# Performance work log

Measured on AMD Instinct MI355X. Metric: run time of the kernel, lower is better.

The kernel has to match this reference:

```python
import jax, jax.numpy as jnp
import numpy as np

N, E, G = 10000, 160000, 64     # nodes, edges, graphs in batch
T, F_IN, F_OUT, L = 5, 75, 15, 4  # towers, per-tower in (divide_input=False), per-tower out, conv layers
AVG_DEG_LOG = float(np.log(17.0))  # stand-in for PyG histogram stat (source deg=zeros -> NaN)
BN_EPS = 1e-5
STD_EPS = 1e-5


def _u(key, shape):
    fi, fo = shape[-2], shape[-1]
    lim = float(np.sqrt(6.0 / (fi + fo)))
    return jax.random.uniform(key, shape, jnp.float32, -lim, lim)


def setup_inputs():
    key = jax.random.key(0)
    k = iter(jax.random.split(key, 24))
    inp = {}
    inp["x"] = jax.random.randint(next(k), (N, 2), 0, 21)
    inp["edge_index"] = jax.random.randint(next(k), (2, E), 0, N)
    inp["edge_attr"] = jax.random.randint(next(k), (E, 2), 0, 4)
    inp["batch"] = jnp.sort(jax.random.randint(next(k), (N,), 0, G))
    inp["node_emb"] = jax.random.normal(next(k), (21, 75), jnp.float32)
    inp["edge_emb"] = jax.random.normal(next(k), (4, 25), jnp.float32)
    inp["pre_lin_W"] = _u(next(k), (150, 75)); inp["pre_lin_b"] = jnp.zeros((75,), jnp.float32)
    inp["edge_enc_W"] = _u(next(k), (L, 50, F_IN)); inp["edge_enc_b"] = jnp.zeros((L, F_IN), jnp.float32)
    inp["pre_W"] = _u(next(k), (L, T, 3 * F_IN, F_IN)); inp["pre_b"] = jnp.zeros((L, T, F_IN), jnp.float32)
    inp["post_W"] = _u(next(k), (L, T, 13 * F_IN, F_OUT)); inp["post_b"] = jnp.zeros((L, T, F_OUT), jnp.float32)
    inp["lin_W"] = _u(next(k), (L, T * F_OUT, 75)); inp["lin_b"] = jnp.zeros((L, 75), jnp.float32)
    inp["bn_g"] = jnp.ones((L, 75), jnp.float32); inp["bn_b"] = jnp.zeros((L, 75), jnp.float32)
    inp["mlp_W1"] = _u(next(k), (75, 50)); inp["mlp_b1"] = jnp.zeros((50,), jnp.float32)
    inp["mlp_W2"] = _u(next(k), (50, 25)); inp["mlp_b2"] = jnp.zeros((25,), jnp.float32)
    inp["mlp_W3"] = _u(next(k), (25, 1)); inp["mlp_b3"] = jnp.zeros((1,), jnp.float32)
    return inp


def _forward(x, edge_index, edge_attr, batch, node_emb, edge_emb, pre_lin_W, pre_lin_b,
             edge_enc_W, edge_enc_b, pre_W, pre_b, post_W, post_b, lin_W, lin_b,
             bn_g, bn_b, mlp_W1, mlp_b1, mlp_W2, mlp_b2, mlp_W3, mlp_b3):
    # node / edge embeddings -> features
    h = node_emb[x].reshape(N, 150) @ pre_lin_W + pre_lin_b          # [N,75]
    ea = edge_emb[edge_attr].reshape(E, 50)                           # [E,50]
    src, dst = edge_index[0], edge_index[1]  # messages flow src -> dst (x_j=src, x_i=dst)

    cnt = jax.ops.segment_sum(jnp.ones((E,), jnp.float32), dst, num_segments=N)  # in-degree [N]
    deg = jnp.maximum(cnt, 1.0)[:, None, None]
    log_deg = jnp.log(jnp.maximum(cnt, 1.0) + 1.0)[:, None, None]
    amp = log_deg / AVG_DEG_LOG
    att = AVG_DEG_LOG / log_deg
    has = (cnt > 0)[:, None, None]

    for l in range(L):
        e = ea @ edge_enc_W[l] + edge_enc_b[l]                        # [E,75]
        m_in = jnp.concatenate([h[dst], h[src], e], axis=-1)          # [E,225]
        msgs = jnp.einsum('ec,tcf->etf', m_in, pre_W[l]) + pre_b[l]   # [E,T,75]
        s = jax.ops.segment_sum(msgs, dst, num_segments=N)
        mean = s / deg
        mean_sq = jax.ops.segment_sum(msgs * msgs, dst, num_segments=N) / deg
        std = jnp.sqrt(jax.nn.relu(mean_sq - mean * mean) + STD_EPS)
        mn = jnp.where(has, jax.ops.segment_min(msgs, dst, num_segments=N), 0.0)
        mx = jnp.where(has, jax.ops.segment_max(msgs, dst, num_segments=N), 0.0)
        agg = jnp.concatenate([mean, mn, mx, std], axis=-1)           # [N,T,300]
        scaled = jnp.concatenate([agg, agg * amp, agg * att], axis=-1)  # [N,T,900]
        out = jnp.concatenate([jnp.broadcast_to(h[:, None, :], (N, T, F_IN)), scaled], axis=-1)  # [N,T,975]
        post = jnp.einsum('ntc,tcf->ntf', out, post_W[l]) + post_b[l]  # [N,T,15]
        hc = post.reshape(N, T * F_OUT) @ lin_W[l] + lin_b[l]          # [N,75]
        mu = hc.mean(axis=0)
        var = hc.var(axis=0)  # biased, matches BatchNorm1d training mode
        h = jax.nn.relu((hc - mu) / jnp.sqrt(var + BN_EPS) * bn_g[l] + bn_b[l])

    g = jax.ops.segment_sum(h, batch, num_segments=G)                 # global_add_pool [G,75]
    g = jax.nn.relu(g @ mlp_W1 + mlp_b1)
    g = jax.nn.relu(g @ mlp_W2 + mlp_b2)
    return g @ mlp_W3 + mlp_b3                                        # [G,1]


def reference(x, edge_index, edge_attr, batch, node_emb, edge_emb, pre_lin_W, pre_lin_b,
              edge_enc_W, edge_enc_b, pre_W, pre_b, post_W, post_b, lin_W, lin_b,
              bn_g, bn_b, mlp_W1, mlp_b1, mlp_W2, mlp_b2, mlp_W3, mlp_b3):
    return _forward(x, edge_index, edge_attr, batch, node_emb, edge_emb, pre_lin_W, pre_lin_b,
                    edge_enc_W, edge_enc_b, pre_W, pre_b, post_W, post_b, lin_W, lin_b,
                    bn_g, bn_b, mlp_W1, mlp_b1, mlp_W2, mlp_b2, mlp_W3, mlp_b3)
```

## Files before the change

### kernel.cpp

```cpp
#include <hip/hip_runtime.h>
#include <hip/hip_bf16.h>
#include <math.h>

#define NN 10000
#define NE 160000
#define NG 64
#define NT 5
#define NL 4
#define ADL 2.833213344056216f
#define AROW 1632

typedef __attribute__((ext_vector_type(8))) short bf16x8;
typedef __attribute__((ext_vector_type(4))) float f32x4;

#define OFF_H      0
#define OFF_HC     750000
#define OFF_P      1500000
#define OFF_Q      5250000
#define OFF_A      9000000
#define OFF_BT     17200000
#define OFF_BIASC  17400000
#define OFF_RLUT   24000000
#define OFF_INVDEG 24006000
#define OFF_AMP    24016000
#define OFF_ATT    24026000
#define OFF_STATS  24036000
#define OFF_GPOOL  24036160
#define OFF_INT    24118960

__device__ __forceinline__ float bf2f(__hip_bfloat16 v){ return __bfloat162float(v); }

__global__ void k_zero_cnt(int* cnt){
    int i = blockIdx.x*256 + threadIdx.x;
    if (i < NN) cnt[i] = 0;
}

__global__ void k_zpad(__hip_bfloat16* __restrict__ A){
    int idx = blockIdx.x*256 + threadIdx.x;
    if (idx >= NN*57) return;
    int n = idx/57, c = idx - n*57;
    int k = (c < 36) ? 1500 + c : 1611 + (c - 36);
    A[(size_t)n*AROW + k] = __float2bfloat16(0.f);
}

__global__ __launch_bounds__(256) void k_h0(const int* __restrict__ x,
        const float* __restrict__ node_emb, const float* __restrict__ plW,
        const float* __restrict__ plb, float* __restrict__ h,
        __hip_bfloat16* __restrict__ A){
    __shared__ float s_emb[21*75];
    __shared__ float s_W[150*75];
    __shared__ float s_b[75];
    int tid = threadIdx.x;
    for (int i = tid; i < 21*75; i += 256) s_emb[i] = node_emb[i];
    for (int i = tid; i < 150*75; i += 256) s_W[i] = plW[i];
    if (tid < 75) s_b[tid] = plb[tid];
    __syncthreads();
    for (int out = blockIdx.x*256 + tid; out < NN*75; out += gridDim.x*256){
        int n = out / 75, f = out - n*75;
        int x0 = x[2*n], x1 = x[2*n+1];
        float acc = s_b[f];
        const float* e0 = s_emb + x0*75;
        const float* e1 = s_emb + x1*75;
        #pragma unroll 5
        for (int k = 0; k < 75; k++)
            acc += e0[k]*s_W[k*75+f] + e1[k]*s_W[(75+k)*75+f];
        h[out] = acc;
        A[(size_t)n*AROW + 1536 + f] = __float2bfloat16(acc);
    }
}

__global__ void k_hist(const int* __restrict__ ei, int* __restrict__ cnt){
    int e = blockIdx.x*256 + threadIdx.x;
    if (e < NE) atomicAdd(&cnt[ei[NE + e]], 1);
}

__global__ void k_scan(const int* __restrict__ cnt, int* __restrict__ eoff){
    __shared__ int buf[256];
    __shared__ int carry;
    int tid = threadIdx.x;
    if (tid == 0){ carry = 0; eoff[0] = 0; }
    __syncthreads();
    for (int base = 0; base < NN; base += 256){
        int v = (base + tid < NN) ? cnt[base + tid] : 0;
        buf[tid] = v; __syncthreads();
        for (int off = 1; off < 256; off <<= 1){
            int t2 = (tid >= off) ? buf[tid - off] : 0;
            __syncthreads();
            buf[tid] += t2;
            __syncthreads();
        }
        int inc = buf[tid] + carry;
        if (base + tid < NN) eoff[base + tid + 1] = inc;
        __syncthreads();
        if (tid == 255) carry = inc;
        __syncthreads();
    }
}

__global__ void k_nodestats(const int* __restrict__ cnt, const int* __restrict__ eoff,
        float* __restrict__ invdeg, float* __restrict__ amp, float* __restrict__ att,
        int* __restrict__ cursor){
    int n = blockIdx.x*256 + threadIdx.x;
    if (n >= NN) return;
    int c = cnt[n];
    cursor[n] = eoff[n];
    float cf = (float)c;
    float dg = cf < 1.f ? 1.f : cf;
    invdeg[n] = 1.f / dg;
    float ld = logf(dg + 1.f);
    amp[n] = ld / ADL;
    att[n] = ADL / ld;
}

__global__ void k_scatter(const int* __restrict__ ei, const int* __restrict__ ea,
        int* __restrict__ cursor, int* __restrict__ esrc, int* __restrict__ ecombo){
    int e = blockIdx.x*256 + threadIdx.x;
    if (e >= NE) return;
    int src = ei[e], dst = ei[NE + e];
    int pos = atomicAdd(&cursor[dst], 1);
    esrc[pos] = src;
    ecombo[pos] = ea[2*e]*4 + ea[2*e+1];
}

__global__ __launch_bounds__(384) void k_pq(const float* __restrict__ h,
        const float* __restrict__ preW, const float* __restrict__ preb,
        const float* __restrict__ edge_emb, const float* __restrict__ encW,
        const float* __restrict__ encb, int l,
        __hip_bfloat16* __restrict__ P, __hip_bfloat16* __restrict__ Q,
        float* __restrict__ Rlut, float* __restrict__ stats){
    __shared__ float smem[10675];
    int tid = threadIdx.x;
    int bx = blockIdx.x;

    if (bx == 318){
        for (int i = tid; i < 150; i += 384) stats[i] = 0.f;
        return;
    }
    if (bx >= 313){
        int t = bx - 313;
        float* s_encW = smem;
        float* s_ev   = smem + 3750;
        float* s_wc   = smem + 4950;
        float* s_ee   = smem + 10575;
        for (int i = tid; i < 3750; i += 384) s_encW[i] = encW[(size_t)l*3750 + i];
        for (int i = tid; i < 100; i += 384) s_ee[i] = edge_emb[i];
        const float* wcsrc = preW + (((size_t)(l*NT + t))*225 + 150)*75;
        for (int i = tid; i < 5625; i += 384) s_wc[i] = wcsrc[i];
        __syncthreads();
        for (int task = tid; task < 1200; task += 384){
            int b = task/75, m = task - 75*b;
            int a0 = b >> 2, a1 = b & 3;
            float s = encb[l*75 + m];
            for (int k = 0; k < 25; k++)
                s += s_ee[a0*25+k]*s_encW[k*75+m] + s_ee[a1*25+k]*s_encW[(25+k)*75+m];
            s_ev[task] = s;
        }
        __syncthreads();
        for (int task = tid; task < 1200; task += 384){
            int b = task/75, f = task - 75*b;
            float r = preb[((size_t)l*NT + t)*75 + f];
            const float* ev = s_ev + b*75;
            #pragma unroll 5
            for (int m = 0; m < 75; m++) r += ev[m]*s_wc[m*75 + f];
            Rlut[b*375 + t*75 + f] = r;
        }
        return;
    }

    float* h_t = smem;
    int base = bx*32;
    for (int idx = tid; idx < 32*75; idx += 384){
        int i = idx/75, m = idx - 75*i;
        int n = base + i;
        h_t[i*76 + m] = (n < NN) ? h[(size_t)n*75 + m] : 0.f;
    }
    __syncthreads();
    int j = tid;
    if (j >= 375) return;
    int t = j/75, f = j - 75*t;
    const float* wbase = preW + ((size_t)(l*NT + t))*225*75 + f;
    float accP[32], accQ[32];
    #pragma unroll
    for (int i = 0; i < 32; i++){ accP[i] = 0.f; accQ[i] = 0.f; }
    for (int m = 0; m < 72; m += 4){
        float wa0 = wbase[(m+0)*75], wa1 = wbase[(m+1)*75];
        float wa2 = wbase[(m+2)*75], wa3 = wbase[(m+3)*75];
        float wb0 = wbase[(75+m+0)*75], wb1 = wbase[(75+m+1)*75];
        float wb2 = wbase[(75+m+2)*75], wb3 = wbase[(75+m+3)*75];
        #pragma unroll
        for (int i = 0; i < 32; i++){
            const float4 hv = *(const float4*)&h_t[i*76 + m];
            accP[i] += hv.x*wa0 + hv.y*wa1 + hv.z*wa2 + hv.w*wa3;
            accQ[i] += hv.x*wb0 + hv.y*wb1 + hv.z*wb2 + hv.w*wb3;
        }
    }
    for (int m = 72; m < 75; m++){
        float wa = wbase[m*75], wb = wbase[(75+m)*75];
        #pragma unroll
        for (int i = 0; i < 32; i++){
            float v = h_t[i*76 + m];
            accP[i] += v*wa; accQ[i] += v*wb;
        }
    }
    for (int i = 0; i < 32; i++){
        int n = base + i;
        if (n < NN){
            P[(size_t)n*375 + j] = __float2bfloat16(accP[i]);
            Q[(size_t)n*375 + j] = __float2bfloat16(accQ[i]);
        }
    }
}

__global__ __launch_bounds__(64) void k_agg(const __hip_bfloat16* __restrict__ P,
        const __hip_bfloat16* __restrict__ Q, const float* __restrict__ Rlut,
        const int* __restrict__ eoff, const int* __restrict__ esrc,
        const int* __restrict__ ecombo, const float* __restrict__ invdeg,
        __hip_bfloat16* __restrict__ A){
    int n = blockIdx.y;
    int j = blockIdx.x*64 + threadIdx.x;
    if (j >= 375) return;
    int lo = eoff[n], hi = eoff[n+1];
    float p = bf2f(P[(size_t)n*375 + j]);
    float sum = 0.f, sq = 0.f, mn = 3.4e38f, mx = -3.4e38f;
    int e = lo;
    for (; e + 8 <= hi; e += 8){
        int s0 = esrc[e],   s1 = esrc[e+1], s2 = esrc[e+2], s3 = esrc[e+3];
        int s4 = esrc[e+4], s5 = esrc[e+5], s6 = esrc[e+6], s7 = esrc[e+7];
        int c0 = ecombo[e],   c1 = ecombo[e+1], c2 = ecombo[e+2], c3 = ecombo[e+3];
        int c4 = ecombo[e+4], c5 = ecombo[e+5], c6 = ecombo[e+6], c7 = ecombo[e+7];
        float q0 = bf2f(Q[(size_t)s0*375 + j]);
        float q1 = bf2f(Q[(size_t)s1*375 + j]);
        float q2 = bf2f(Q[(size_t)s2*375 + j]);
        float q3 = bf2f(Q[(size_t)s3*375 + j]);
        float q4 = bf2f(Q[(size_t)s4*375 + j]);
        float q5 = bf2f(Q[(size_t)s5*375 + j]);
        float q6 = bf2f(Q[(size_t)s6*375 + j]);
        float q7 = bf2f(Q[(size_t)s7*375 + j]);
        float r0 = Rlut[c0*375 + j], r1 = Rlut[c1*375 + j];
        float r2 = Rlut[c2*375 + j], r3 = Rlut[c3*375 + j];
        float r4 = Rlut[c4*375 + j], r5 = Rlut[c5*375 + j];
        float r6 = Rlut[c6*375 + j], r7 = Rlut[c7*375 + j];
        float m0 = p + q0 + r0, m1 = p + q1 + r1;
        float m2 = p + q2 + r2, m3 = p + q3 + r3;
        float m4 = p + q4 + r4, m5 = p + q5 + r5;
        float m6 = p + q6 + r6, m7 = p + q7 + r7;
        sum += (m0 + m1 + m2 + m3) + (m4 + m5 + m6 + m7);
        sq  += (m0*m0 + m1*m1 + m2*m2 + m3*m3) + (m4*m4 + m5*m5 + m6*m6 + m7*m7);
        mn = fminf(mn, fminf(fminf(fminf(m0,m1), fminf(m2,m3)),
                             fminf(fminf(m4,m5), fminf(m6,m7))));
        mx = fmaxf(mx, fmaxf(fmaxf(fmaxf(m0,m1), fmaxf(m2,m3)),
                             fmaxf(fmaxf(m4,m5), fmaxf(m6,m7))));
    }
    for (; e < hi; e++){
        int s = esrc[e], cm = ecombo[e];
        float m = p + bf2f(Q[(size_t)s*375 + j]) + Rlut[cm*375 + j];
        sum += m; sq += m*m;
        mn = fminf(mn, m); mx = fmaxf(mx, m);
    }
    float id = invdeg[n];
    bool has = hi > lo;
    float mean = sum*id;
    float msq  = sq*id;
    float var = msq - mean*mean; var = var > 0.f ? var : 0.f;
    float sd = sqrtf(var + 1e-5f);
    float mnv = has ? mn : 0.f;
    float mxv = has ? mx : 0.f;
    int t = j/75, f = j - 75*t;
    __hip_bfloat16* a = A + (size_t)n*AROW + t*300;
    a[f]      = __float2bfloat16(mean);
    a[75+f]   = __float2bfloat16(mnv);
    a[150+f]  = __float2bfloat16(mxv);
    a[225+f]  = __float2bfloat16(sd);
}

__global__ __launch_bounds__(256) void k_prep(const float* __restrict__ postW,
        const float* __restrict__ postb, const float* __restrict__ linW,
        const float* __restrict__ linb, int l,
        __hip_bfloat16* __restrict__ BT, float* __restrict__ biasc){
    int tid = threadIdx.x;
    if (blockIdx.x == 1530){
        if (tid < 80){
            float s = (tid < 75) ? linb[l*75 + tid] : 0.f;
            if (tid < 75)
                for (int tf = 0; tf < 75; tf++)
                    s += postb[l*75 + tf]*linW[(size_t)l*5625 + tf*75 + tid];
            biasc[tid] = s;
        }
        return;
    }
    __shared__ float s_lin[5625];
    for (int i = tid; i < 5625; i += 256) s_lin[i] = linW[(size_t)l*5625 + i];
    __syncthreads();
    int idx = blockIdx.x*256 + tid;
    int mat = idx / (80*AROW);
    int rem = idx - mat*(80*AROW);
    int o = rem / AROW;
    int k = rem - o*AROW;
    float v = 0.f;
    if (o < 75){
        if (k < 1500){
            int t = k / 300, kk = k - t*300;
            int c = (mat == 0 ? 75 : (mat == 1 ? 375 : 675)) + kk;
            const float* pw = postW + (((size_t)(l*NT + t))*975 + c)*15;
            const float* lw = s_lin + t*15*75 + o;
            #pragma unroll
            for (int f = 0; f < 15; f++) v += pw[f]*lw[f*75];
        } else if (k >= 1536 && k < 1611 && mat == 0){
            int c = k - 1536;
            for (int t = 0; t < 5; t++){
                const float* pw = postW + (((size_t)(l*NT + t))*975 + c)*15;
                const float* lw = s_lin + t*15*75 + o;
                #pragma unroll
                for (int f = 0; f < 15; f++) v += pw[f]*lw[f*75];
            }
        }
    }
    BT[idx] = __float2bfloat16(v);
}

__global__ __launch_bounds__(256) void k_gemm(const __hip_bfloat16* __restrict__ A,
        const __hip_bfloat16* __restrict__ BT, const float* __restrict__ biasc,
        const float* __restrict__ amp, const float* __restrict__ att,
        float* __restrict__ hc, float* __restrict__ stats){
    __shared__ float scratch[4*16*80];
    __shared__ float comb[3*16*80];
    int tid = threadIdx.x;
    int wave = tid >> 6;
    int lane = tid & 63;
    int nb = blockIdx.x;
    int mrow = lane & 15;
    int q = lane >> 4;
    int n0 = nb*16;

    f32x4 acc[3][5];
    #pragma unroll
    for (int mt = 0; mt < 3; mt++)
        #pragma unroll
        for (int nt = 0; nt < 5; nt++)
            acc[mt][nt] = (f32x4){0.f, 0.f, 0.f, 0.f};

    int k0 = wave*13;
    int k1 = (wave == 3) ? 51 : k0 + 13;
    const __hip_bfloat16* arow_p = A + (size_t)(n0 + mrow)*AROW + q*8;
    for (int ks = k0; ks < k1; ks++){
        bf16x8 afrag = *(const bf16x8*)(arow_p + (size_t)ks*32);
        #pragma unroll
        for (int mt = 0; mt < 3; mt++){
            const __hip_bfloat16* bbase = BT + ((size_t)mt*80 + mrow)*AROW + q*8 + (size_t)ks*32;
            #pragma unroll
            for (int nt = 0; nt < 5; nt++){
                bf16x8 bfrag = *(const bf16x8*)(bbase + (size_t)nt*16*AROW);
                acc[mt][nt] = __builtin_amdgcn_mfma_f32_16x16x32_bf16(
                                  afrag, bfrag, acc[mt][nt], 0, 0, 0);
            }
        }
    }
    for (int mt = 0; mt < 3; mt++){
        #pragma unroll
        for (int nt = 0; nt < 5; nt++)
            #pragma unroll
            for (int r = 0; r < 4; r++)
                scratch[(wave*16 + q*4 + r)*80 + nt*16 + (lane & 15)] = acc[mt][nt][r];
        __syncthreads();
        for (int i = tid; i < 16*80; i += 256)
            comb[mt*1280 + i] = scratch[i] + scratch[1280 + i]
                              + scratch[2560 + i] + scratch[3840 + i];
        __syncthreads();
    }
    for (int i = tid; i < 16*80; i += 256){
        int r = i / 80, o = i - r*80;
        int n = n0 + r;
        float v = comb[i] + amp[n]*comb[1280 + i] + att[n]*comb[2560 + i] + biasc[o];
        scratch[i] = v;
        if (o < 75) hc[(size_t)n*75 + o] = v;
    }
    __syncthreads();
    if (tid < 75){
        float s1 = 0.f, s2 = 0.f;
        #pragma unroll
        for (int r = 0; r < 16; r++){
            float v = scratch[r*80 + tid];
            s1 += v; s2 += v*v;
        }
        atomicAdd(&stats[tid], s1);
        atomicAdd(&stats[75 + tid], s2);
    }
}

__global__ void k_bnapply(const float* __restrict__ hc, const float* __restrict__ stats,
        const float* __restrict__ bng, const float* __restrict__ bnb, int l,
        float* __restrict__ h, __hip_bfloat16* __restrict__ A){
    int idx = blockIdx.x*256 + threadIdx.x;
    if (idx >= NN*75) return;
    int col = idx % 75;
    int n = idx / 75;
    float mu = stats[col]*(1.0f/NN);
    float var = stats[75+col]*(1.0f/NN) - mu*mu;
    float inv = rsqrtf(var + 1e-5f);
    float v = (hc[idx] - mu)*inv*bng[l*75+col] + bnb[l*75+col];
    v = v > 0.f ? v : 0.f;
    h[idx] = v;
    A[(size_t)n*AROW + 1536 + col] = __float2bfloat16(v);
}

__global__ __launch_bounds__(256) void k_pool(const float* __restrict__ h,
        const int* __restrict__ batch, float* __restrict__ gpool){
    int g = blockIdx.x, tid = threadIdx.x;
    int lo = 0, hi = NN;
    while (lo < hi){ int mid = (lo+hi)>>1; if (batch[mid] < g) lo = mid+1; else hi = mid; }
    int start = lo;
    lo = start; hi = NN;
    while (lo < hi){ int mid = (lo+hi)>>1; if (batch[mid] < g+1) lo = mid+1; else hi = mid; }
    int end = lo;
    __shared__ float red[225];
    if (tid < 225){
        int col = tid % 75, rep = tid / 75;
        float acc = 0.f;
        for (int i = start + rep; i < end; i += 3) acc += h[(size_t)i*75 + col];
        red[tid] = acc;
    }
    __syncthreads();
    if (tid < 75) gpool[g*75 + tid] = red[tid] + red[75+tid] + red[150+tid];
}

__global__ __launch_bounds__(256) void k_mlp(const float* __restrict__ gpool,
        const float* __restrict__ W1, const float* __restrict__ b1,
        const float* __restrict__ W2, const float* __restrict__ b2,
        const float* __restrict__ W3, const float* __restrict__ b3,
        float* __restrict__ out){
    __shared__ float w1[75*50];
    __shared__ float w2[50*25];
    __shared__ float gp[8*75];
    __shared__ float t1[8*50];
    __shared__ float t2[8*25];
    int tid = threadIdx.x;
    int gbase = blockIdx.x*8;
    for (int i = tid; i < 75*50; i += 256) w1[i] = W1[i];
    for (int i = tid; i < 50*25; i += 256) w2[i] = W2[i];
    for (int i = tid; i < 8*75; i += 256) gp[i] = gpool[gbase*75 + i];
    __syncthreads();
    for (int task = tid; task < 8*50; task += 256){
        int g = task/50, j = task - 50*g;
        float s = b1[j];
        const float* gv = gp + g*75;
        #pragma unroll 5
        for (int k = 0; k < 75; k++) s += gv[k]*w1[k*50+j];
        t1[task] = s > 0.f ? s : 0.f;
    }
    __syncthreads();
    for (int task = tid; task < 8*25; task += 256){
        int g = task/25, j = task - 25*g;
        float s = b2[j];
        const float* tv = t1 + g*50;
        #pragma unroll 5
        for (int k = 0; k < 50; k++) s += tv[k]*w2[k*25+j];
        t2[task] = s > 0.f ? s : 0.f;
    }
    __syncthreads();
    if (tid < 8){
        float s = b3[0];
        const float* tv = t2 + tid*25;
        #pragma unroll
        for (int k = 0; k < 25; k++) s += tv[k]*W3[k];
        out[gbase + tid] = s;
    }
}

extern "C" void kernel_launch(void* const* d_in, const int* in_sizes, int n_in,
                              void* d_out, int out_size, void* d_ws, size_t ws_size,
                              hipStream_t stream){
    const int* x          = (const int*)d_in[0];
    const int* edge_index = (const int*)d_in[1];
    const int* edge_attr  = (const int*)d_in[2];
    const int* batch      = (const int*)d_in[3];
    const float* node_emb = (const float*)d_in[4];
    const float* edge_emb = (const float*)d_in[5];
    const float* pre_lin_W= (const float*)d_in[6];
    const float* pre_lin_b= (const float*)d_in[7];
    const float* encW     = (const float*)d_in[8];
    const float* encb     = (const float*)d_in[9];
    const float* preW     = (const float*)d_in[10];
    const float* preb     = (const float*)d_in[11];
    const float* postW    = (const float*)d_in[12];
    const float* postb    = (const float*)d_in[13];
    const float* linW     = (const float*)d_in[14];
    const float* linb     = (const float*)d_in[15];
    const float* bng      = (const float*)d_in[16];
    const float* bnb      = (const float*)d_in[17];
    const float* mlpW1    = (const float*)d_in[18];
    const float* mlpb1    = (const float*)d_in[19];
    const float* mlpW2    = (const float*)d_in[20];
    const float* mlpb2    = (const float*)d_in[21];
    const float* mlpW3    = (const float*)d_in[22];
    const float* mlpb3    = (const float*)d_in[23];

    float* ws = (float*)d_ws;
    float* h      = ws + OFF_H;
    float* hc     = ws + OFF_HC;
    __hip_bfloat16* P = (__hip_bfloat16*)(ws + OFF_P);
    __hip_bfloat16* Q = (__hip_bfloat16*)(ws + OFF_Q);
    __hip_bfloat16* A = (__hip_bfloat16*)(ws + OFF_A);
    __hip_bfloat16* BT = (__hip_bfloat16*)(ws + OFF_BT);
    float* biasc  = ws + OFF_BIASC;
    float* Rlut   = ws + OFF_RLUT;
    float* invdeg = ws + OFF_INVDEG;
    float* amp    = ws + OFF_AMP;
    float* att    = ws + OFF_ATT;
    float* stats  = ws + OFF_STATS;
    float* gpool  = ws + OFF_GPOOL;
    int* iw     = (int*)(ws + OFF_INT);
    int* cnt    = iw;
    int* eoff   = cnt + NN;
    int* cursor = eoff + NN + 2;
    int* esrc   = cursor + NN;
    int* ecombo = esrc + NE;

    k_zero_cnt<<<40, 256, 0, stream>>>(cnt);
    k_zpad<<<(NN*57 + 255)/256, 256, 0, stream>>>(A);
    k_h0<<<640, 256, 0, stream>>>(x, node_emb, pre_lin_W, pre_lin_b, h, A);
    k_hist<<<625, 256, 0, stream>>>(edge_index, cnt);
    k_scan<<<1, 256, 0, stream>>>(cnt, eoff);
    k_nodestats<<<40, 256, 0, stream>>>(cnt, eoff, invdeg, amp, att, cursor);
    k_scatter<<<625, 256, 0, stream>>>(edge_index, edge_attr, cursor, esrc, ecombo);

    for (int l = 0; l < NL; l++){
        k_pq<<<319, 384, 0, stream>>>(h, preW, preb, edge_emb, encW, encb, l,
                                      P, Q, Rlut, stats);
        k_agg<<<dim3(6, NN), 64, 0, stream>>>(P, Q, Rlut, eoff, esrc, ecombo, invdeg, A);
        k_prep<<<1531, 256, 0, stream>>>(postW, postb, linW, linb, l, BT, biasc);
        k_gemm<<<625, 256, 0, stream>>>(A, BT, biasc, amp, att, hc, stats);
        k_bnapply<<<2930, 256, 0, stream>>>(hc, stats, bng, bnb, l, h, A);
    }

    k_pool<<<NG, 256, 0, stream>>>(h, batch, gpool);
    k_mlp<<<8, 256, 0, stream>>>(gpool, mlpW1, mlpb1, mlpW2, mlpb2, mlpW3, mlpb3, (float*)d_out);
}
```

Before: 951.3 us.

## Tile GEMM through LDS with 32-row blocks, hoist weight prep, split BN stats

The node GEMM now stages 32 rows of A and all 240 rows of BT through shared memory in 128-wide K chunks. Each wave computes two 16-row M tiles, which improves reuse of B fragments; the old version had each wave read B directly from global memory. The per-layer weight folding (k_prep) is hoisted out of the layer loop into four launches up front, with separate BT and bias buffers per layer. BatchNorm statistics move out of the GEMM epilogue into a separate k_bnstats kernel that uses shared-memory atomics. In exchange there is an extra launch per layer and an extra read of hc, and 313 blocks leave fewer blocks in flight on the GPU.

```diff
diff --git a/kernel.cpp b/kernel.cpp
--- a/kernel.cpp
+++ b/kernel.cpp
@@ -9,6 +9,7 @@
 #define NL 4
 #define ADL 2.833213344056216f
 #define AROW 1632
+#define BTL  391680
 
 typedef __attribute__((ext_vector_type(8))) short bf16x8;
 typedef __attribute__((ext_vector_type(4))) float f32x4;
@@ -19,7 +20,7 @@
 #define OFF_Q      5250000
 #define OFF_A      9000000
 #define OFF_BT     17200000
-#define OFF_BIASC  17400000
+#define OFF_BIASC  18000000
 #define OFF_RLUT   24000000
 #define OFF_INVDEG 24006000
 #define OFF_AMP    24016000
@@ -318,73 +319,113 @@
     BT[idx] = __float2bfloat16(v);
 }
 
-__global__ __launch_bounds__(256) void k_gemm(const __hip_bfloat16* __restrict__ A,
+#define SBF 136
+__global__ __launch_bounds__(256, 2) void k_gemm(const __hip_bfloat16* __restrict__ A,
         const __hip_bfloat16* __restrict__ BT, const float* __restrict__ biasc,
         const float* __restrict__ amp, const float* __restrict__ att,
-        float* __restrict__ hc, float* __restrict__ stats){
-    __shared__ float scratch[4*16*80];
-    __shared__ float comb[3*16*80];
-    int tid = threadIdx.x;
-    int wave = tid >> 6;
-    int lane = tid & 63;
-    int nb = blockIdx.x;
-    int mrow = lane & 15;
-    int q = lane >> 4;
-    int n0 = nb*16;
-
-    f32x4 acc[3][5];
+        float* __restrict__ hc){
+    __shared__ short smem_s[272*SBF];
+    __hip_bfloat16* sA = (__hip_bfloat16*)smem_s;
+    __hip_bfloat16* sB = (__hip_bfloat16*)smem_s + 32*SBF;
+    float* scratch = (float*)smem_s;
+    int tid = threadIdx.x;
+    int wave = tid >> 6, lane = tid & 63;
+    int fr = lane & 15, q = lane >> 4;
+    int n0 = blockIdx.x*32;
+
+    f32x4 acc[2][3][5];
     #pragma unroll
-    for (int mt = 0; mt < 3; mt++)
+    for (int mt = 0; mt < 2; mt++)
         #pragma unroll
-        for (int nt = 0; nt < 5; nt++)
-            acc[mt][nt] = (f32x4){0.f, 0.f, 0.f, 0.f};
-
-    int k0 = wave*13;
-    int k1 = (wave == 3) ? 51 : k0 + 13;
-    const __hip_bfloat16* arow_p = A + (size_t)(n0 + mrow)*AROW + q*8;
-    for (int ks = k0; ks < k1; ks++){
-        bf16x8 afrag = *(const bf16x8*)(arow_p + (size_t)ks*32);
+        for (int mat = 0; mat < 3; mat++)
+            #pragma unroll
+            for (int nt = 0; nt < 5; nt++)
+                acc[mt][mat][nt] = (f32x4){0.f, 0.f, 0.f, 0.f};
+
+    const bf16x8 zv = (bf16x8){0,0,0,0,0,0,0,0};
+    for (int kbase = 0; kbase < 1632; kbase += 128){
+        __syncthreads();
+        for (int idx = tid; idx < 32*16; idx += 256){
+            int row = idx >> 4, seg = idx & 15;
+            int n = n0 + row, k = kbase + seg*8;
+            bf16x8 v = zv;
+            if (n < NN && k < 1632) v = *(const bf16x8*)(A + (size_t)n*AROW + k);
+            *(bf16x8*)(sA + row*SBF + seg*8) = v;
+        }
+        for (int idx = tid; idx < 240*16; idx += 256){
+            int row = idx >> 4, seg = idx & 15;
+            int k = kbase + seg*8;
+            bf16x8 v = zv;
+            if (k < 1632) v = *(const bf16x8*)(BT + (size_t)row*AROW + k);
+            *(bf16x8*)(sB + row*SBF + seg*8) = v;
+        }
+        __syncthreads();
+        int kk = wave*32;
+        if (kbase + kk < 1632){
+            bf16x8 a0 = *(const bf16x8*)(sA + fr*SBF + kk + q*8);
+            bf16x8 a1 = *(const bf16x8*)(sA + (16 + fr)*SBF + kk + q*8);
+            #pragma unroll
+            for (int mat = 0; mat < 3; mat++)
+                #pragma unroll
+                for (int nt = 0; nt < 5; nt++){
+                    bf16x8 b = *(const bf16x8*)(sB + (mat*80 + nt*16 + fr)*SBF + kk + q*8);
+                    acc[0][mat][nt] = __builtin_amdgcn_mfma_f32_16x16x32_bf16(
+                                          a0, b, acc[0][mat][nt], 0, 0, 0);
+                    acc[1][mat][nt] = __builtin_amdgcn_mfma_f32_16x16x32_bf16(
+                                          a1, b, acc[1][mat][nt], 0, 0, 0);
+                }
+        }
+    }
+
+    float part[10];
+    #pragma unroll
+    for (int j = 0; j < 10; j++){
+        int i = tid + j*256;
+        part[j] = biasc[i - (i/80)*80];
+    }
+    for (int mat = 0; mat < 3; mat++){
+        __syncthreads();
         #pragma unroll
-        for (int mt = 0; mt < 3; mt++){
-            const __hip_bfloat16* bbase = BT + ((size_t)mt*80 + mrow)*AROW + q*8 + (size_t)ks*32;
+        for (int mt = 0; mt < 2; mt++)
             #pragma unroll
-            for (int nt = 0; nt < 5; nt++){
-                bf16x8 bfrag = *(const bf16x8*)(bbase + (size_t)nt*16*AROW);
-                acc[mt][nt] = __builtin_amdgcn_mfma_f32_16x16x32_bf16(
-                                  afrag, bfrag, acc[mt][nt], 0, 0, 0);
-            }
-        }
-    }
-    for (int mt = 0; mt < 3; mt++){
+            for (int nt = 0; nt < 5; nt++)
+                #pragma unroll
+                for (int r = 0; r < 4; r++)
+                    scratch[wave*2560 + (mt*16 + q*4 + r)*80 + nt*16 + fr]
+                        = acc[mt][mat][nt][r];
+        __syncthreads();
         #pragma unroll
-        for (int nt = 0; nt < 5; nt++)
-            #pragma unroll
-            for (int r = 0; r < 4; r++)
-                scratch[(wave*16 + q*4 + r)*80 + nt*16 + (lane & 15)] = acc[mt][nt][r];
-        __syncthreads();
-        for (int i = tid; i < 16*80; i += 256)
-            comb[mt*1280 + i] = scratch[i] + scratch[1280 + i]
-                              + scratch[2560 + i] + scratch[3840 + i];
-        __syncthreads();
-    }
-    for (int i = tid; i < 16*80; i += 256){
-        int r = i / 80, o = i - r*80;
-        int n = n0 + r;
-        float v = comb[i] + amp[n]*comb[1280 + i] + att[n]*comb[2560 + i] + biasc[o];
-        scratch[i] = v;
-        if (o < 75) hc[(size_t)n*75 + o] = v;
-    }
-    __syncthreads();
-    if (tid < 75){
-        float s1 = 0.f, s2 = 0.f;
-        #pragma unroll
-        for (int r = 0; r < 16; r++){
-            float v = scratch[r*80 + tid];
-            s1 += v; s2 += v*v;
-        }
-        atomicAdd(&stats[tid], s1);
-        atomicAdd(&stats[75 + tid], s2);
-    }
+        for (int j = 0; j < 10; j++){
+            int i = tid + j*256;
+            int n = n0 + i/80;
+            float s = scratch[i] + scratch[2560 + i] + scratch[5120 + i] + scratch[7680 + i];
+            float coef = 1.f;
+            if (mat == 1) coef = (n < NN) ? amp[n] : 0.f;
+            if (mat == 2) coef = (n < NN) ? att[n] : 0.f;
+            part[j] += coef*s;
+        }
+    }
+    #pragma unroll
+    for (int j = 0; j < 10; j++){
+        int i = tid + j*256;
+        int n = n0 + i/80, o = i - (i/80)*80;
+        if (n < NN && o < 75) hc[(size_t)n*75 + o] = part[j];
+    }
+}
+
+__global__ void k_bnstats(const float* __restrict__ hc, float* __restrict__ stats){
+    __shared__ float part[150];
+    int tid = threadIdx.x;
+    if (tid < 150) part[tid] = 0.f;
+    __syncthreads();
+    for (size_t idx = blockIdx.x*256 + tid; idx < (size_t)NN*75; idx += (size_t)gridDim.x*256){
+        float v = hc[idx];
+        int col = (int)(idx % 75);
+        atomicAdd(&part[col], v);
+        atomicAdd(&part[75 + col], v*v);
+    }
+    __syncthreads();
+    if (tid < 150) atomicAdd(&stats[tid], part[tid]);
 }
 
 __global__ void k_bnapply(const float* __restrict__ hc, const float* __restrict__ stats,
@@ -522,13 +563,17 @@
     k_scan<<<1, 256, 0, stream>>>(cnt, eoff);
     k_nodestats<<<40, 256, 0, stream>>>(cnt, eoff, invdeg, amp, att, cursor);
     k_scatter<<<625, 256, 0, stream>>>(edge_index, edge_attr, cursor, esrc, ecombo);
+    for (int l = 0; l < NL; l++)
+        k_prep<<<1531, 256, 0, stream>>>(postW, postb, linW, linb, l,
+                                         BT + (size_t)l*BTL, biasc + l*80);
 
     for (int l = 0; l < NL; l++){
         k_pq<<<319, 384, 0, stream>>>(h, preW, preb, edge_emb, encW, encb, l,
                                       P, Q, Rlut, stats);
         k_agg<<<dim3(6, NN), 64, 0, stream>>>(P, Q, Rlut, eoff, esrc, ecombo, invdeg, A);
-        k_prep<<<1531, 256, 0, stream>>>(postW, postb, linW, linb, l, BT, biasc);
-        k_gemm<<<625, 256, 0, stream>>>(A, BT, biasc, amp, att, hc, stats);
+        k_gemm<<<313, 256, 0, stream>>>(A, BT + (size_t)l*BTL, biasc + l*80,
+                                        amp, att, hc);
+        k_bnstats<<<128, 256, 0, stream>>>(hc, stats);
         k_bnapply<<<2930, 256, 0, stream>>>(hc, stats, bng, bnb, l, h, A);
     }
 
```

Measured after the change: 1.035 ms. +8.8%, slower.
